# Performance work log

Measured on AMD Instinct MI355X. Metric: run time of the kernel, lower is better.

Reference implementation:

```python
import jax, jax.numpy as jnp
import numpy as np

BN_EPS = 1e-5


def three_nn(unknown, known):
    # squared pairwise distances via gemm form: ||u||^2 + ||k||^2 - 2 u.k
    # unknown: (B, n, 3), known: (B, m, 3) -> d: (B, n, m)
    u2 = jnp.sum(unknown * unknown, axis=-1, keepdims=True)          # (B, n, 1)
    k2 = jnp.sum(known * known, axis=-1)[:, None, :]                 # (B, 1, m)
    d = u2 + k2 - 2.0 * jnp.einsum('bnc,bmc->bnm', unknown, known)   # (B, n, m)
    neg_d, idx = jax.lax.top_k(-d, 3)                                # 3 smallest
    return -neg_d, idx                                               # (B,n,3), (B,n,3) int32


def three_interpolate(known_feats, idx, weight):
    # known_feats: (B, C, m), idx/weight: (B, n, 3) -> (B, C, n)
    g = jnp.take_along_axis(known_feats[:, :, None, :], idx[:, None, :, :], axis=3)  # (B,C,n,3)
    return jnp.sum(g * weight[:, None, :, :], axis=3)


def conv1x1(x, W, b):
    # x: (B, C_in, N), W: (C_out, C_in), b: (C_out,)
    return jnp.einsum('oc,bcn->bon', W, x) + b[None, :, None]


def batchnorm(x, gamma, beta):
    # training-mode BN over (B, N) per channel, biased variance
    mean = jnp.mean(x, axis=(0, 2), keepdims=True)
    var = jnp.mean((x - mean) ** 2, axis=(0, 2), keepdims=True)
    xn = (x - mean) * jax.lax.rsqrt(var + BN_EPS)
    return xn * gamma[None, :, None] + beta[None, :, None]


def setup_inputs() -> dict:
    key = jax.random.key(0)
    ks = jax.random.split(key, 16)
    B, n, m = 16, 4096, 1024
    C1, C2, C = 128, 256, 256  # in_channels, known feat channels (=mlp[0]), mlp width
    inp = {
        'unknown': jax.random.normal(ks[0], (B, n, 3), jnp.float32),
        'known': jax.random.normal(ks[1], (B, m, 3), jnp.float32),
        'unknow_feats': jax.random.normal(ks[2], (B, C1, n), jnp.float32),
        'known_feats': jax.random.normal(ks[3], (B, C2, m), jnp.float32),
        # mlp_unknow: Conv1d(C1->C) + BN (no relu)
        'Wu': jax.random.normal(ks[4], (C, C1), jnp.float32) * (1.0 / np.sqrt(C1)),
        'bu': jnp.zeros((C,), jnp.float32),
        'gu': jnp.ones((C,), jnp.float32),
        'betau': jnp.zeros((C,), jnp.float32),
        # mlp_convs[0]: Conv1d(C->C) + BN + relu
        'W1': jax.random.normal(ks[5], (C, C), jnp.float32) * (1.0 / np.sqrt(C)),
        'b1': jnp.zeros((C,), jnp.float32),
        'g1': jnp.ones((C,), jnp.float32),
        'beta1': jnp.zeros((C,), jnp.float32),
        # mlp_convs[1]: Conv1d(C->C) + BN + relu
        'W2': jax.random.normal(ks[6], (C, C), jnp.float32) * (1.0 / np.sqrt(C)),
        'b2': jnp.zeros((C,), jnp.float32),
        'g2': jnp.ones((C,), jnp.float32),
        'beta2': jnp.zeros((C,), jnp.float32),
    }
    return inp


def reference(unknown, known, unknow_feats, known_feats,
              Wu, bu, gu, betau, W1, b1, g1, beta1, W2, b2, g2, beta2):
    dist, idx = three_nn(unknown, known)            # squared dists (B,n,3)
    dist_recip = 1.0 / (dist + 1e-8)
    norm = jnp.sum(dist_recip, axis=2, keepdims=True)
    weight = dist_recip / norm
    interpolated = three_interpolate(known_feats, idx, weight)   # (B, 256, n)

    skip = batchnorm(conv1x1(unknow_feats, Wu, bu), gu, betau)   # (B, 256, n)
    x = interpolated + skip
    x = jax.nn.relu(batchnorm(conv1x1(x, W1, b1), g1, beta1))
    x = jax.nn.relu(batchnorm(conv1x1(x, W2, b2), g2, beta2))
    return x
```

## Files before the change

kernel.cpp:

```cpp
#include <hip/hip_runtime.h>
#include <hip/hip_bf16.h>
#include <cstddef>
#include <cstdint>

#define BATCH 16
#define NPTS  4096
#define MPTS  1024
#define PTOT  65536
#define C1    128
#define C2    256

typedef short bf16x8 __attribute__((ext_vector_type(8)));
typedef float f32x4  __attribute__((ext_vector_type(4)));

static __device__ __forceinline__ float bf2f(unsigned int u16) {
    union { unsigned int i; float f; } v; v.i = u16 << 16; return v.f;
}
static __device__ __forceinline__ unsigned short f2bf(float f) {
    union { float f; unsigned int i; } v; v.f = f;
    unsigned int u = v.i;
    return (unsigned short)((u + 0x7FFFu + ((u >> 16) & 1u)) >> 16);
}


template <int SWZ>
__global__ void k_transpose(const float* __restrict__ in, unsigned short* __restrict__ out,
                            int C, int N) {
    __shared__ float tile[64][65];
    int b  = blockIdx.z;
    int n0 = blockIdx.x * 64;
    int c0 = blockIdx.y * 64;
    const float* src = in + (size_t)b * C * N;
    unsigned short* dst = out + (size_t)b * N * C;
    int t  = threadIdx.x;
    int t4 = t >> 6;
    int tn = t & 63;
#pragma unroll
    for (int i = 0; i < 16; ++i) {
        int cc = i * 4 + t4;
        tile[cc][tn] = src[(size_t)(c0 + cc) * N + n0 + tn];
    }
    __syncthreads();
#pragma unroll
    for (int i = 0; i < 16; ++i) {
        int nn = i * 4 + t4;
        int p  = n0 + nn;
        int c  = c0 + tn;
        size_t off;
        if (SWZ) off = (size_t)p * C + (size_t)((((c >> 3) ^ (p & 7)) << 3) + (c & 7));
        else     off = (size_t)p * C + c;
        dst[off] = f2bf(tile[tn][nn]);
    }
}

__global__ void k_cvt(const float* __restrict__ in, unsigned short* __restrict__ out, int n) {
    int i = blockIdx.x * 256 + threadIdx.x;
    if (i < n) out[i] = f2bf(in[i]);
}

static __device__ __forceinline__ bool nn_less(float da, int ia, float db, int ib) {
    return (da < db) || (da == db && ia < ib);
}

__global__ void k_three_nn(const float* __restrict__ unknown, const float* __restrict__ known,
                           int* __restrict__ idx_out, float* __restrict__ w_out) {
    __shared__ float4 kpt[MPTS + 4];
    int t  = threadIdx.x;
    int p0 = blockIdx.x * 64;
    int b  = p0 >> 12;
    const float* kb = known + (size_t)b * MPTS * 3;
    for (int i = t; i < MPTS; i += 256) {
        float x = kb[i * 3 + 0], y = kb[i * 3 + 1], z = kb[i * 3 + 2];
        float dd = __fadd_rn(__fadd_rn(__fmul_rn(x, x), __fmul_rn(y, y)), __fmul_rn(z, z));
        float4 v; v.x = x; v.y = y; v.z = z; v.w = dd;
        kpt[i + (i >> 8)] = v;
    }
    __syncthreads();

    int q = t & 3;
    int p = p0 + (t >> 2);
    const float* up = unknown + (size_t)p * 3;
    float ux = up[0], uy = up[1], uz = up[2];
    float u2 = __fadd_rn(__fadd_rn(__fmul_rn(ux, ux), __fmul_rn(uy, uy)), __fmul_rn(uz, uz));

    float d0 = INFINITY, d1 = INFINITY, d2 = INFINITY;
    int   i0 = 0, i1 = 0, i2 = 0;
    int base = q * 257;
#pragma unroll 4
    for (int it = 0; it < 256; ++it) {
        float4 kp = kpt[base + it];
        float dot = __fadd_rn(__fadd_rn(__fmul_rn(ux, kp.x), __fmul_rn(uy, kp.y)),
                              __fmul_rn(uz, kp.z));
        float d = __fsub_rn(__fadd_rn(u2, kp.w), __fmul_rn(2.0f, dot));
        int k = q * 256 + it;
        if (d < d0)      { d2 = d1; i2 = i1; d1 = d0; i1 = i0; d0 = d; i0 = k; }
        else if (d < d1) { d2 = d1; i2 = i1; d1 = d;  i1 = k; }
        else if (d < d2) { d2 = d;  i2 = k; }
    }

#pragma unroll
    for (int m = 1; m <= 2; m <<= 1) {
        float e0 = __shfl_xor(d0, m, 64), e1 = __shfl_xor(d1, m, 64), e2 = __shfl_xor(d2, m, 64);
        int   j0 = __shfl_xor(i0, m, 64), j1 = __shfl_xor(i1, m, 64), j2 = __shfl_xor(i2, m, 64);
        float a0 = d0, a1 = d1, a2 = d2; int x0 = i0, x1 = i1, x2 = i2;
        float b0 = e0, b1 = e1, b2 = e2; int y0 = j0, y1 = j1, y2 = j2;
        bool tk = nn_less(a0, x0, b0, y0);
        d0 = tk ? a0 : b0; i0 = tk ? x0 : y0;
        float na0 = tk ? a1 : a0; int nx0 = tk ? x1 : x0;
        float na1 = tk ? a2 : a1; int nx1 = tk ? x2 : x1;
        float nb0 = tk ? b0 : b1; int ny0 = tk ? y0 : y1;
        float nb1 = tk ? b1 : b2; int ny1 = tk ? y1 : y2;
        tk = nn_less(na0, nx0, nb0, ny0);
        d1 = tk ? na0 : nb0; i1 = tk ? nx0 : ny0;
        float ma0 = tk ? na1 : na0; int mx0 = tk ? nx1 : nx0;
        float mb0 = tk ? nb0 : nb1; int my0 = tk ? ny0 : ny1;
        tk = nn_less(ma0, mx0, mb0, my0);
        d2 = tk ? ma0 : mb0; i2 = tk ? mx0 : my0;
    }

    if (q == 0) {
        float r0 = 1.0f / (d0 + 1e-8f), r1 = 1.0f / (d1 + 1e-8f), r2 = 1.0f / (d2 + 1e-8f);
        float norm = r0 + r1 + r2;
        size_t pg = (size_t)p;
        idx_out[pg * 3 + 0] = i0; idx_out[pg * 3 + 1] = i1; idx_out[pg * 3 + 2] = i2;
        w_out[pg * 3 + 0] = r0 / norm; w_out[pg * 3 + 1] = r1 / norm; w_out[pg * 3 + 2] = r2 / norm;
    }
}

template <int K, int APPLY>
__global__ __launch_bounds__(256, 2) void k_gemm(
        const unsigned short* __restrict__ Wb,
        const unsigned short* __restrict__ X,
        const float* __restrict__ bias,
        const float* __restrict__ aff_a,
        const float* __restrict__ aff_c,
        unsigned short* __restrict__ Y,
        float* __restrict__ partial) {
    constexpr int RED_BYTES  = 2 * 16 * 257 * 4;
    constexpr int TILE_BYTES = 64 * K * 2;
    constexpr int SMEM_BYTES = TILE_BYTES > RED_BYTES ? TILE_BYTES : RED_BYTES;
    __shared__ char smem[SMEM_BYTES];

    const int t    = threadIdx.x;
    const int p0   = blockIdx.x * 64;
    const int wv   = t >> 6;
    const int lane = t & 63;
    const int lhi  = lane >> 4, llo = lane & 15;

    if (!APPLY) {
        const char* src = (const char*)(X + (size_t)p0 * K);
        constexpr int ITERS = TILE_BYTES / (256 * 16);
#pragma unroll
        for (int i = 0; i < ITERS; ++i) {
            int off = (i * 256 + t) * 16;
            __builtin_amdgcn_global_load_lds(
                (const __attribute__((address_space(1))) unsigned int*)(src + off),
                (__attribute__((address_space(3))) unsigned int*)(smem + off),
                16, 0, 0);
        }
    } else {
        constexpr int CPR = K / 8;
#pragma unroll
        for (int i = 0; i < (64 * CPR) / 256; ++i) {
            int f   = i * 256 + t;
            int row = f / CPR, qp = f % CPR;
            int col = qp ^ (row & 7);
            uint4 v = *(const uint4*)(X + (size_t)(p0 + row) * K + qp * 8);
            unsigned int w[4] = {v.x, v.y, v.z, v.w};
            float4 a0 = *(const float4*)(aff_a + col * 8);
            float4 a1 = *(const float4*)(aff_a + col * 8 + 4);
            float4 cc0 = *(const float4*)(aff_c + col * 8);
            float4 cc1 = *(const float4*)(aff_c + col * 8 + 4);
            float aa[8] = {a0.x, a0.y, a0.z, a0.w, a1.x, a1.y, a1.z, a1.w};
            float cc[8] = {cc0.x, cc0.y, cc0.z, cc0.w, cc1.x, cc1.y, cc1.z, cc1.w};
#pragma unroll
            for (int q2 = 0; q2 < 4; ++q2) {
                float lo = fmaxf(bf2f(w[q2] & 0xffff) * aa[q2 * 2]     + cc[q2 * 2],     0.0f);
                float hi = fmaxf(bf2f(w[q2] >> 16)    * aa[q2 * 2 + 1] + cc[q2 * 2 + 1], 0.0f);
                w[q2] = (unsigned int)f2bf(lo) | ((unsigned int)f2bf(hi) << 16);
            }
            uint4 o; o.x = w[0]; o.y = w[1]; o.z = w[2]; o.w = w[3];
            *(uint4*)(smem + row * (K * 2) + qp * 16) = o;
        }
    }

    bf16x8 wf[K / 32][4];
#pragma unroll
    for (int ks = 0; ks < K / 32; ++ks)
#pragma unroll
        for (int i = 0; i < 4; ++i) {
            int ch = wv * 64 + i * 16 + llo;
            wf[ks][i] = *(const bf16x8*)(Wb + (size_t)ch * K + ks * 32 + lhi * 8);
        }

    __syncthreads();

    f32x4 acc[4][4];
#pragma unroll
    for (int i = 0; i < 4; ++i)
#pragma unroll
        for (int j = 0; j < 4; ++j) acc[i][j] = (f32x4){0.f, 0.f, 0.f, 0.f};

#pragma unroll
    for (int ks = 0; ks < K / 32; ++ks) {
        bf16x8 bb[4];
#pragma unroll
        for (int j = 0; j < 4; ++j) {
            int row = j * 16 + llo;
            int cp  = (ks * 4 + lhi) ^ (row & 7);
            bb[j] = *(const bf16x8*)(smem + row * (K * 2) + cp * 16);
        }
#pragma unroll
        for (int i = 0; i < 4; ++i)
#pragma unroll
            for (int j = 0; j < 4; ++j)
                acc[i][j] = __builtin_amdgcn_mfma_f32_16x16x32_bf16(wf[ks][i], bb[j], acc[i][j], 0, 0, 0);
    }

    float s[4][4], sq[4][4];
#pragma unroll
    for (int i = 0; i < 4; ++i) {
        int cbase = wv * 64 + i * 16 + lhi * 4;
        float4 bv = *(const float4*)(bias + cbase);
        int c8 = cbase >> 3, hf = lhi & 1;
#pragma unroll
        for (int e = 0; e < 4; ++e) { s[i][e] = 0.f; sq[i][e] = 0.f; }
#pragma unroll
        for (int j = 0; j < 4; ++j) {
            int p = p0 + j * 16 + llo;
            float y0 = acc[i][j][0] + bv.x;
            float y1 = acc[i][j][1] + bv.y;
            float y2 = acc[i][j][2] + bv.z;
            float y3 = acc[i][j][3] + bv.w;
            s[i][0] += y0; sq[i][0] += y0 * y0;
            s[i][1] += y1; sq[i][1] += y1 * y1;
            s[i][2] += y2; sq[i][2] += y2 * y2;
            s[i][3] += y3; sq[i][3] += y3 * y3;
            unsigned int lo = (unsigned int)f2bf(y0) | ((unsigned int)f2bf(y1) << 16);
            unsigned int hi = (unsigned int)f2bf(y2) | ((unsigned int)f2bf(y3) << 16);
            uint2 o; o.x = lo; o.y = hi;
            *(uint2*)(Y + (size_t)p * 256 + ((c8 ^ (p & 7)) << 3) + hf * 4) = o;
        }
    }

    __syncthreads();
    float* red = (float*)smem;
#pragma unroll
    for (int i = 0; i < 4; ++i) {
        int cbase = wv * 64 + i * 16 + lhi * 4;
#pragma unroll
        for (int e = 0; e < 4; ++e) {
            red[llo * 257 + cbase + e]            = s[i][e];
            red[16 * 257 + llo * 257 + cbase + e] = sq[i][e];
        }
    }
    __syncthreads();
    {
        float ssum = 0.f, qsum = 0.f;
#pragma unroll 4
        for (int l = 0; l < 16; ++l) {
            ssum += red[l * 257 + t];
            qsum += red[16 * 257 + l * 257 + t];
        }
        partial[(size_t)blockIdx.x * 512 + t]       = ssum;
        partial[(size_t)blockIdx.x * 512 + 256 + t] = qsum;
    }
}

__global__ void k_red1(const float* __restrict__ partial, float* __restrict__ partA) {
    int t = threadIdx.x, g = blockIdx.x;
    float s = 0.f, q = 0.f;
#pragma unroll
    for (int i = 0; i < 16; ++i) {
        const float* pp = partial + (size_t)(g * 16 + i) * 512;
        s += pp[t]; q += pp[256 + t];
    }
    partA[g * 512 + t]       = s;
    partA[g * 512 + 256 + t] = q;
}

__global__ void k_finalize(const float* __restrict__ partA, const float* __restrict__ gamma,
                           const float* __restrict__ beta, float* __restrict__ aff_a,
                           float* __restrict__ aff_c) {
    int c = threadIdx.x;
    float s = 0.f, q = 0.f;
#pragma unroll 8
    for (int i = 0; i < 64; ++i) { s += partA[i * 512 + c]; q += partA[i * 512 + 256 + c]; }
    float mean = s * (1.0f / PTOT);
    float var  = fmaxf(q * (1.0f / PTOT) - mean * mean, 0.0f);
    float a    = gamma[c] / sqrtf(var + 1e-5f);
    aff_a[c] = a;
    aff_c[c] = beta[c] - mean * a;
}

__global__ void k_build_x(const unsigned short* __restrict__ y0, const unsigned short* __restrict__ kfT,
                          const int* __restrict__ idx, const float* __restrict__ wgt,
                          const float* __restrict__ aff_a, const float* __restrict__ aff_c,
                          unsigned short* __restrict__ X) {
    int t   = threadIdx.x;
    int p   = blockIdx.x * 8 + (t >> 5);
    int col = t & 31;
    int c0  = col * 8;
    int b   = p >> 12;
    int pos = col ^ (p & 7);
    int i0 = idx[p * 3 + 0], i1 = idx[p * 3 + 1], i2 = idx[p * 3 + 2];
    float w0 = wgt[p * 3 + 0], w1 = wgt[p * 3 + 1], w2 = wgt[p * 3 + 2];
    const size_t kb = (size_t)b * MPTS * C2;
    uint4 v0 = *(const uint4*)(kfT + kb + (size_t)i0 * C2 + c0);
    uint4 v1 = *(const uint4*)(kfT + kb + (size_t)i1 * C2 + c0);
    uint4 v2 = *(const uint4*)(kfT + kb + (size_t)i2 * C2 + c0);
    uint4 vy = *(const uint4*)(y0 + (size_t)p * C2 + pos * 8);
    const unsigned int* u0 = (const unsigned int*)&v0;
    const unsigned int* u1 = (const unsigned int*)&v1;
    const unsigned int* u2 = (const unsigned int*)&v2;
    const unsigned int* uy = (const unsigned int*)&vy;
    unsigned int r[4];
#pragma unroll
    for (int q = 0; q < 4; ++q) {
        int c = c0 + q * 2;
        float lo = w0 * bf2f(u0[q] & 0xffff) + w1 * bf2f(u1[q] & 0xffff) + w2 * bf2f(u2[q] & 0xffff)
                 + bf2f(uy[q] & 0xffff) * aff_a[c] + aff_c[c];
        float hi = w0 * bf2f(u0[q] >> 16) + w1 * bf2f(u1[q] >> 16) + w2 * bf2f(u2[q] >> 16)
                 + bf2f(uy[q] >> 16) * aff_a[c + 1] + aff_c[c + 1];
        r[q] = (unsigned int)f2bf(lo) | ((unsigned int)f2bf(hi) << 16);
    }
    uint4 vout; vout.x = r[0]; vout.y = r[1]; vout.z = r[2]; vout.w = r[3];
    *(uint4*)(X + (size_t)p * C2 + pos * 8) = vout;
}

__global__ void k_final(const unsigned short* __restrict__ Y2, const float* __restrict__ aff_a,
                        const float* __restrict__ aff_c, float* __restrict__ out) {
    __shared__ float tile[64][65];
    int p0 = blockIdx.x * 64;
    int c0 = blockIdx.y * 64;
    int t  = threadIdx.x;
    int t4 = t >> 6, t64 = t & 63;
#pragma unroll
    for (int i = 0; i < 16; ++i) {
        int r = i * 4 + t4;
        int p = p0 + r;
        int c = c0 + t64;
        float v = bf2f(Y2[(size_t)p * 256 + (((c >> 3) ^ (p & 7)) << 3) + (c & 7)])
                  * aff_a[c] + aff_c[c];
        tile[t64][r] = fmaxf(v, 0.0f);
    }
    __syncthreads();
    int b   = p0 >> 12;
    int pin = p0 & 4095;
#pragma unroll
    for (int i = 0; i < 16; ++i) {
        int cc = i * 4 + t4;
        out[((size_t)b * 256 + c0 + cc) * 4096 + pin + t64] = tile[cc][t64];
    }
}

extern "C" void kernel_launch(void* const* d_in, const int* in_sizes, int n_in,
                              void* d_out, int out_size, void* d_ws, size_t ws_size,
                              hipStream_t stream) {
    const float* unknown = (const float*)d_in[0];
    const float* known   = (const float*)d_in[1];
    const float* ufeat   = (const float*)d_in[2];
    const float* kfeat   = (const float*)d_in[3];
    const float* Wu      = (const float*)d_in[4];
    const float* bu      = (const float*)d_in[5];
    const float* gu      = (const float*)d_in[6];
    const float* betau   = (const float*)d_in[7];
    const float* W1      = (const float*)d_in[8];
    const float* b1      = (const float*)d_in[9];
    const float* g1      = (const float*)d_in[10];
    const float* beta1   = (const float*)d_in[11];
    const float* W2      = (const float*)d_in[12];
    const float* b2      = (const float*)d_in[13];
    const float* g2      = (const float*)d_in[14];
    const float* beta2   = (const float*)d_in[15];
    float* out = (float*)d_out;

    char* ws = (char*)d_ws;
    unsigned short* reg0 = (unsigned short*)ws;
    unsigned short* ybuf = (unsigned short*)(ws + ((size_t)32 << 20));
    unsigned short* kfT  = (unsigned short*)(ws + ((size_t)64 << 20));
    unsigned short* Wub  = (unsigned short*)(ws + ((size_t)72 << 20));
    unsigned short* W1b  = Wub + 256 * 128;
    unsigned short* W2b  = W1b + 256 * 256;
    int*   idxb = (int*)(W2b + 256 * 256);
    float* wgtb = (float*)(idxb + (size_t)PTOT * 3);
    float* affa0 = wgtb + (size_t)PTOT * 3;
    float* affc0 = affa0 + 256;
    float* affa1 = affc0 + 256;
    float* affc1 = affa1 + 256;
    float* affa2 = affc1 + 256;
    float* affc2 = affa2 + 256;
    float* part0  = (float*)(ws + ((size_t)16 << 20));
    float* partA0 = (float*)(ws + ((size_t)18 << 20));
    float* part12  = (float*)(ws + ((size_t)64 << 20));
    float* partA12 = (float*)(ws + ((size_t)66 << 20));
    if (ws_size < ((size_t)75 << 20)) return;

    k_transpose<1><<<dim3(NPTS / 64, C1 / 64, BATCH), 256, 0, stream>>>(ufeat, reg0, C1, NPTS);
    k_transpose<0><<<dim3(MPTS / 64, C2 / 64, BATCH), 256, 0, stream>>>(kfeat, kfT, C2, MPTS);
    k_cvt<<<(256 * 128 + 255) / 256, 256, 0, stream>>>(Wu, Wub, 256 * 128);
    k_cvt<<<(256 * 256 + 255) / 256, 256, 0, stream>>>(W1, W1b, 256 * 256);
    k_cvt<<<(256 * 256 + 255) / 256, 256, 0, stream>>>(W2, W2b, 256 * 256);

    k_three_nn<<<PTOT / 64, 256, 0, stream>>>(unknown, known, idxb, wgtb);

    k_gemm<C1, 0><<<PTOT / 64, 256, 0, stream>>>(Wub, reg0, bu, nullptr, nullptr, ybuf, part0);
    k_red1<<<64, 256, 0, stream>>>(part0, partA0);
    k_finalize<<<1, 256, 0, stream>>>(partA0, gu, betau, affa0, affc0);

    k_build_x<<<PTOT / 8, 256, 0, stream>>>(ybuf, kfT, idxb, wgtb, affa0, affc0, reg0);

    k_gemm<C2, 0><<<PTOT / 64, 256, 0, stream>>>(W1b, reg0, b1, nullptr, nullptr, ybuf, part12);
    k_red1<<<64, 256, 0, stream>>>(part12, partA12);
    k_finalize<<<1, 256, 0, stream>>>(partA12, g1, beta1, affa1, affc1);

    k_gemm<C2, 1><<<PTOT / 64, 256, 0, stream>>>(W2b, ybuf, b2, affa1, affc1, reg0, part12);
    k_red1<<<64, 256, 0, stream>>>(part12, partA12);
    k_finalize<<<1, 256, 0, stream>>>(partA12, g2, beta2, affa2, affc2);

    k_final<<<dim3(PTOT / 64, 4), 256, 0, stream>>>(reg0, affa2, affc2, out);

    (void)in_sizes; (void)n_in; (void)out_size;
}
```

Baseline: 225.6 us.

## Pre-pack weights into MFMA fragment order, double-buffer weight loads, and stage outputs through LDS

Result: faster. 211.3 us (-6.3%).

```diff
diff --git a/kernel.cpp b/kernel.cpp
--- a/kernel.cpp
+++ b/kernel.cpp
@@ -53,9 +53,14 @@
     }
 }
 
-__global__ void k_cvt(const float* __restrict__ in, unsigned short* __restrict__ out, int n) {
-    int i = blockIdx.x * 256 + threadIdx.x;
-    if (i < n) out[i] = f2bf(in[i]);
+__global__ void k_cvt_pack(const float* __restrict__ in, unsigned short* __restrict__ out, int K) {
+    int tid = blockIdx.x * 256 + threadIdx.x;
+    if (tid >= 256 * K) return;
+    int ch = tid / K, k = tid % K;
+    int ks = k >> 5, lhi = (k >> 3) & 3, e = k & 7;
+    int wv = ch >> 6, i = (ch >> 4) & 3, llo = ch & 15;
+    int lane = lhi * 16 + llo;
+    out[((size_t)((ks * 16 + wv * 4 + i) * 64 + lane)) * 8 + e] = f2bf(in[tid]);
 }
 
 static __device__ __forceinline__ bool nn_less(float da, int ia, float db, int ib) {
@@ -128,17 +133,17 @@
 }
 
 template <int K, int APPLY>
-__global__ __launch_bounds__(256, 2) void k_gemm(
-        const unsigned short* __restrict__ Wb,
+__global__ void k_gemm(
+        const unsigned short* __restrict__ Wp,
         const unsigned short* __restrict__ X,
         const float* __restrict__ bias,
         const float* __restrict__ aff_a,
         const float* __restrict__ aff_c,
         unsigned short* __restrict__ Y,
         float* __restrict__ partial) {
-    constexpr int RED_BYTES  = 2 * 16 * 257 * 4;
+    constexpr int NK = K / 32;
     constexpr int TILE_BYTES = 64 * K * 2;
-    constexpr int SMEM_BYTES = TILE_BYTES > RED_BYTES ? TILE_BYTES : RED_BYTES;
+    constexpr int SMEM_BYTES = TILE_BYTES > 32768 ? TILE_BYTES : 32768;
     __shared__ char smem[SMEM_BYTES];
 
     const int t    = threadIdx.x;
@@ -184,14 +189,11 @@
         }
     }
 
-    bf16x8 wf[K / 32][4];
-#pragma unroll
-    for (int ks = 0; ks < K / 32; ++ks)
-#pragma unroll
-        for (int i = 0; i < 4; ++i) {
-            int ch = wv * 64 + i * 16 + llo;
-            wf[ks][i] = *(const bf16x8*)(Wb + (size_t)ch * K + ks * 32 + lhi * 8);
-        }
+    const unsigned short* wbase = Wp + ((size_t)(wv * 4 * 64) + lane) * 8;
+    bf16x8 wA[4], wB[4];
+#pragma unroll
+    for (int i = 0; i < 4; ++i)
+        wA[i] = *(const bf16x8*)(wbase + i * 512);
 
     __syncthreads();
 
@@ -202,68 +204,90 @@
         for (int j = 0; j < 4; ++j) acc[i][j] = (f32x4){0.f, 0.f, 0.f, 0.f};
 
 #pragma unroll
-    for (int ks = 0; ks < K / 32; ++ks) {
-        bf16x8 bb[4];
-#pragma unroll
-        for (int j = 0; j < 4; ++j) {
-            int row = j * 16 + llo;
-            int cp  = (ks * 4 + lhi) ^ (row & 7);
-            bb[j] = *(const bf16x8*)(smem + row * (K * 2) + cp * 16);
-        }
+    for (int ks = 0; ks < NK; ks += 2) {
 #pragma unroll
         for (int i = 0; i < 4; ++i)
-#pragma unroll
-            for (int j = 0; j < 4; ++j)
-                acc[i][j] = __builtin_amdgcn_mfma_f32_16x16x32_bf16(wf[ks][i], bb[j], acc[i][j], 0, 0, 0);
-    }
-
-    float s[4][4], sq[4][4];
+            wB[i] = *(const bf16x8*)(wbase + (size_t)(ks + 1) * 8192 + i * 512);
+        {
+            bf16x8 bb[4];
+#pragma unroll
+            for (int j = 0; j < 4; ++j) {
+                int row = j * 16 + llo;
+                int cp  = (ks * 4 + lhi) ^ (row & 7);
+                bb[j] = *(const bf16x8*)(smem + row * (K * 2) + cp * 16);
+            }
+#pragma unroll
+            for (int i = 0; i < 4; ++i)
+#pragma unroll
+                for (int j = 0; j < 4; ++j)
+                    acc[i][j] = __builtin_amdgcn_mfma_f32_16x16x32_bf16(wA[i], bb[j], acc[i][j], 0, 0, 0);
+        }
+        if (ks + 2 < NK) {
+#pragma unroll
+            for (int i = 0; i < 4; ++i)
+                wA[i] = *(const bf16x8*)(wbase + (size_t)(ks + 2) * 8192 + i * 512);
+        }
+        {
+            bf16x8 bb[4];
+#pragma unroll
+            for (int j = 0; j < 4; ++j) {
+                int row = j * 16 + llo;
+                int cp  = ((ks + 1) * 4 + lhi) ^ (row & 7);
+                bb[j] = *(const bf16x8*)(smem + row * (K * 2) + cp * 16);
+            }
+#pragma unroll
+            for (int i = 0; i < 4; ++i)
+#pragma unroll
+                for (int j = 0; j < 4; ++j)
+                    acc[i][j] = __builtin_amdgcn_mfma_f32_16x16x32_bf16(wB[i], bb[j], acc[i][j], 0, 0, 0);
+        }
+    }
+
+    __syncthreads();
 #pragma unroll
     for (int i = 0; i < 4; ++i) {
         int cbase = wv * 64 + i * 16 + lhi * 4;
         float4 bv = *(const float4*)(bias + cbase);
         int c8 = cbase >> 3, hf = lhi & 1;
-#pragma unroll
-        for (int e = 0; e < 4; ++e) { s[i][e] = 0.f; sq[i][e] = 0.f; }
+        float s0 = 0.f, s1 = 0.f, s2 = 0.f, s3 = 0.f;
+        float q0 = 0.f, q1 = 0.f, q2 = 0.f, q3 = 0.f;
 #pragma unroll
         for (int j = 0; j < 4; ++j) {
-            int p = p0 + j * 16 + llo;
+            int row = j * 16 + llo;
             float y0 = acc[i][j][0] + bv.x;
             float y1 = acc[i][j][1] + bv.y;
             float y2 = acc[i][j][2] + bv.z;
             float y3 = acc[i][j][3] + bv.w;
-            s[i][0] += y0; sq[i][0] += y0 * y0;
-            s[i][1] += y1; sq[i][1] += y1 * y1;
-            s[i][2] += y2; sq[i][2] += y2 * y2;
-            s[i][3] += y3; sq[i][3] += y3 * y3;
+            s0 += y0; q0 += y0 * y0;  s1 += y1; q1 += y1 * y1;
+            s2 += y2; q2 += y2 * y2;  s3 += y3; q3 += y3 * y3;
             unsigned int lo = (unsigned int)f2bf(y0) | ((unsigned int)f2bf(y1) << 16);
             unsigned int hi = (unsigned int)f2bf(y2) | ((unsigned int)f2bf(y3) << 16);
             uint2 o; o.x = lo; o.y = hi;
-            *(uint2*)(Y + (size_t)p * 256 + ((c8 ^ (p & 7)) << 3) + hf * 4) = o;
-        }
-    }
-
-    __syncthreads();
-    float* red = (float*)smem;
-#pragma unroll
-    for (int i = 0; i < 4; ++i) {
-        int cbase = wv * 64 + i * 16 + lhi * 4;
-#pragma unroll
-        for (int e = 0; e < 4; ++e) {
-            red[llo * 257 + cbase + e]            = s[i][e];
-            red[16 * 257 + llo * 257 + cbase + e] = sq[i][e];
+            *(uint2*)(smem + row * 512 + ((c8 ^ (row & 7)) << 4) + hf * 8) = o;
+        }
+#pragma unroll
+        for (int m = 1; m <= 8; m <<= 1) {
+            s0 += __shfl_xor(s0, m, 64); q0 += __shfl_xor(q0, m, 64);
+            s1 += __shfl_xor(s1, m, 64); q1 += __shfl_xor(q1, m, 64);
+            s2 += __shfl_xor(s2, m, 64); q2 += __shfl_xor(q2, m, 64);
+            s3 += __shfl_xor(s3, m, 64); q3 += __shfl_xor(q3, m, 64);
+        }
+        if (llo == 0) {
+            float4 sv; sv.x = s0; sv.y = s1; sv.z = s2; sv.w = s3;
+            float4 qv; qv.x = q0; qv.y = q1; qv.z = q2; qv.w = q3;
+            *(float4*)(partial + (size_t)blockIdx.x * 512 + cbase)       = sv;
+            *(float4*)(partial + (size_t)blockIdx.x * 512 + 256 + cbase) = qv;
         }
     }
     __syncthreads();
     {
-        float ssum = 0.f, qsum = 0.f;
-#pragma unroll 4
-        for (int l = 0; l < 16; ++l) {
-            ssum += red[l * 257 + t];
-            qsum += red[16 * 257 + l * 257 + t];
-        }
-        partial[(size_t)blockIdx.x * 512 + t]       = ssum;
-        partial[(size_t)blockIdx.x * 512 + 256 + t] = qsum;
+        const char* ysrc = smem + wv * 8192 + lane * 16;
+        char* ydst = (char*)(Y + (size_t)p0 * 256) + wv * 8192 + lane * 16;
+#pragma unroll
+        for (int i2 = 0; i2 < 8; ++i2) {
+            uint4 v = *(const uint4*)(ysrc + i2 * 1024);
+            *(uint4*)(ydst + i2 * 1024) = v;
+        }
     }
 }
 
@@ -398,9 +422,9 @@
 
     k_transpose<1><<<dim3(NPTS / 64, C1 / 64, BATCH), 256, 0, stream>>>(ufeat, reg0, C1, NPTS);
     k_transpose<0><<<dim3(MPTS / 64, C2 / 64, BATCH), 256, 0, stream>>>(kfeat, kfT, C2, MPTS);
-    k_cvt<<<(256 * 128 + 255) / 256, 256, 0, stream>>>(Wu, Wub, 256 * 128);
-    k_cvt<<<(256 * 256 + 255) / 256, 256, 0, stream>>>(W1, W1b, 256 * 256);
-    k_cvt<<<(256 * 256 + 255) / 256, 256, 0, stream>>>(W2, W2b, 256 * 256);
+    k_cvt_pack<<<(256 * 128 + 255) / 256, 256, 0, stream>>>(Wu, Wub, 128);
+    k_cvt_pack<<<(256 * 256 + 255) / 256, 256, 0, stream>>>(W1, W1b, 256);
+    k_cvt_pack<<<(256 * 256 + 255) / 256, 256, 0, stream>>>(W2, W2b, 256);
 
     k_three_nn<<<PTOT / 64, 256, 0, stream>>>(unknown, known, idxb, wgtb);
 
```
